# Kernel optimization log

Measured on AMD Instinct MI355X. Metric: run time of the kernel, lower is better.

Reference implementation:

```python
import jax, jax.numpy as jnp
import numpy as np

N = 100000       # nodes
E = 1600000      # edges
F_IN = 128       # input features
HID = 64         # hidden dim
CLS = 16         # classes


def setup_inputs() -> dict:
    key = jax.random.key(0)
    k = jax.random.split(key, 6)
    x = jax.random.normal(k[0], (N, F_IN), dtype=jnp.float32)
    src = jax.random.randint(k[1], (E,), 0, N, dtype=jnp.int32)
    dst = jax.random.randint(k[2], (E,), 0, N, dtype=jnp.int32)
    edge_index = jnp.stack([src, dst], axis=0)
    W1 = jax.random.normal(k[3], (F_IN, HID), dtype=jnp.float32) * (1.0 / np.sqrt(F_IN))
    b1 = jnp.zeros((HID,), dtype=jnp.float32)
    W2 = jax.random.normal(k[4], (HID, CLS), dtype=jnp.float32) * (1.0 / np.sqrt(HID))
    b2 = jnp.zeros((CLS,), dtype=jnp.float32)
    return {"x": x, "edge_index": edge_index, "W1": W1, "b1": b1, "W2": W2, "b2": b2}


def gcn_conv(x, W, b, src, dst, n_nodes):
    # GCNConv(normalize=True): h = W x; out_i = sum_{j->i} h_j / sqrt(d_i d_j) + h_i / d_i + b
    # (self-loops added with weight 1; deg includes the self-loop)
    h = x @ W                                             # [N, out]
    ones = jnp.ones(src.shape[0], dtype=x.dtype)
    deg = jax.ops.segment_sum(ones, dst, num_segments=n_nodes) + 1.0   # [N]
    dinv = deg ** -0.5
    norm = dinv[src] * dinv[dst]                          # [E]
    msg = h[src] * norm[:, None]                          # [E, out] gather
    out = jax.ops.segment_sum(msg, dst, num_segments=n_nodes)          # scatter-add
    out = out + h * (1.0 / deg)[:, None] + b              # self-loop term + bias
    return out


def reference(x, edge_index, W1, b1, W2, b2):
    src, dst = edge_index[0], edge_index[1]
    n = x.shape[0]
    h = jax.nn.relu(gcn_conv(x, W1, b1, src, dst, n))
    # dropout(p=0.5) is identity in eval mode
    h = jax.nn.relu(gcn_conv(h, W2, b2, src, dst, n))
    return jax.nn.log_softmax(h, axis=-1)
```

## Files before the change

kernel.cpp:

```cpp
#include <hip/hip_runtime.h>
#include <hip/hip_bf16.h>


typedef unsigned short u16;
typedef __attribute__((ext_vector_type(8))) short short8;
typedef __attribute__((ext_vector_type(4))) float f32x4;

#define CAP 4096

__device__ __forceinline__ float bf2f(u16 u) {
  return __uint_as_float(((unsigned int)u) << 16);
}
__device__ __forceinline__ u16 f2bf(float f) {
  unsigned int u = __float_as_uint(f);
  u += 0x7fffu + ((u >> 16) & 1u);
  return (u16)(u >> 16);
}
__device__ __forceinline__ float blo(unsigned int u) {
  return __uint_as_float(u << 16);
}
__device__ __forceinline__ float bhi(unsigned int u) {
  return __uint_as_float(u & 0xffff0000u);
}

__global__ __launch_bounds__(512) void kpartc(
    const int* __restrict__ src, const int* __restrict__ dst,
    int* __restrict__ cursor, int* __restrict__ etmp,
    const void* __restrict__ W1r, const void* __restrict__ b1r,
    const void* __restrict__ W2r, const void* __restrict__ b2r,
    u16* __restrict__ W1t, float* __restrict__ b1f, u16* __restrict__ W2b,
    float* __restrict__ b2f, int* __restrict__ mode, int E, int NB) {
  __shared__ int hist[1024], basep[1024];
  __shared__ float red[8];
  __shared__ int smode;
  int tid = threadIdx.x;

  if (blockIdx.x == 0) {
    const u16* w = (const u16*)W1r;
    float mx = 0.f;
    for (int i = tid; i < 8192; i += 512) {
      float av = fabsf(bf2f(w[i]));
      if (!(av <= 1e6f)) av = 3e38f;
      mx = fmaxf(mx, av);
    }
    #pragma unroll
    for (int off = 32; off >= 1; off >>= 1) mx = fmaxf(mx, __shfl_xor(mx, off, 64));
    if ((tid & 63) == 0) red[tid >> 6] = mx;
    __syncthreads();
    if (tid == 0) {
      float m2 = 0.f;
      #pragma unroll
      for (int wv = 0; wv < 8; ++wv) m2 = fmaxf(m2, red[wv]);
      smode = (m2 > 1e6f) ? 1 : 0;
      mode[0] = smode;
    }
    __syncthreads();
    int m = smode;
    for (int i = tid; i < 8192; i += 512) {
      int f = i >> 9, l = (i >> 3) & 63, j = i & 7;
      int k = (f >> 2) * 32 + (l >> 4) * 8 + j;
      int n = (f & 3) * 16 + (l & 15);
      int s = k * 64 + n;
      W1t[i] = m ? f2bf(((const float*)W1r)[s]) : ((const u16*)W1r)[s];
    }
    for (int i = tid; i < 1024; i += 512)
      W2b[i] = m ? f2bf(((const float*)W2r)[i]) : ((const u16*)W2r)[i];
    if (tid < 64) b1f[tid] = m ? ((const float*)b1r)[tid] : bf2f(((const u16*)b1r)[tid]);
    if (tid < 16) b2f[tid] = m ? ((const float*)b2r)[tid] : bf2f(((const u16*)b2r)[tid]);
    return;
  }

  for (int i = tid; i < 1024; i += 512) hist[i] = 0;
  __syncthreads();
  int e0 = (blockIdx.x - 1) * 8192 + tid * 16;
  int pk[16], off[16], cb[16];
  if (e0 + 15 < E) {
    int4 s4[4], d4[4];
    #pragma unroll
    for (int u = 0; u < 4; ++u) {
      s4[u] = ((const int4*)(src + e0))[u];
      d4[u] = ((const int4*)(dst + e0))[u];
    }
    const int* sp = (const int*)s4;
    const int* dp = (const int*)d4;
    #pragma unroll
    for (int k = 0; k < 16; ++k) {
      int s = sp[k], d = dp[k];
      cb[k] = d >> 7;
      pk[k] = (s << 7) | (d & 127);
      off[k] = atomicAdd(&hist[cb[k]], 1);
    }
  } else {
    #pragma unroll
    for (int k = 0; k < 16; ++k) {
      int e = e0 + k;
      cb[k] = -1;
      if (e < E) {
        int s = src[e], d = dst[e];
        cb[k] = d >> 7;
        pk[k] = (s << 7) | (d & 127);
        off[k] = atomicAdd(&hist[cb[k]], 1);
      }
    }
  }
  __syncthreads();
  for (int i = tid; i < NB; i += 512)
    if (hist[i]) basep[i] = atomicAdd(&cursor[i], hist[i]);
  __syncthreads();
  if (e0 + 15 < E) {
    #pragma unroll
    for (int k = 0; k < 16; ++k)
      etmp[cb[k] * CAP + basep[cb[k]] + off[k]] = pk[k];
  } else {
    #pragma unroll
    for (int k = 0; k < 16; ++k)
      if (cb[k] >= 0) etmp[cb[k] * CAP + basep[cb[k]] + off[k]] = pk[k];
  }
}

__global__ __launch_bounds__(256) void ksort(
    const int* __restrict__ etmp, const int* __restrict__ cursor,
    float* __restrict__ dinv, int* __restrict__ esort,
    int2* __restrict__ rowse, int N) {
  __shared__ int hist[128], curs[128];
  int tid = threadIdx.x;
  int bk = blockIdx.x;
  int base = bk * CAP;
  int cnt = cursor[bk];
  int node0 = bk << 7;

  if (tid < 128) hist[tid] = 0;
  __syncthreads();
  for (int i = tid; i < cnt; i += 256)
    atomicAdd(&hist[etmp[base + i] & 127], 1);
  __syncthreads();
  if (tid < 64) {
    int v0 = hist[tid], v1 = hist[tid + 64];
    int s0 = v0;
    #pragma unroll
    for (int off = 1; off < 64; off <<= 1) {
      int t = __shfl_up(s0, off, 64);
      if (tid >= off) s0 += t;
    }
    int tot0 = __shfl(s0, 63, 64);
    int s1 = v1;
    #pragma unroll
    for (int off = 1; off < 64; off <<= 1) {
      int t = __shfl_up(s1, off, 64);
      if (tid >= off) s1 += t;
    }
    s1 += tot0;
    int e0x = s0 - v0, e1x = s1 - v1;
    curs[tid] = e0x;
    curs[tid + 64] = e1x;
    int n0 = node0 + tid, n1 = n0 + 64;
    if (n0 < N) {
      rowse[n0] = make_int2(base + e0x, base + e0x + v0);
      dinv[n0] = rsqrtf((float)(v0 + 1));
    }
    if (n1 < N) {
      rowse[n1] = make_int2(base + e1x, base + e1x + v1);
      dinv[n1] = rsqrtf((float)(v1 + 1));
    }
  }
  __syncthreads();
  for (int i = tid; i < cnt; i += 256) {
    int pk = etmp[base + i];
    int pos = atomicAdd(&curs[pk & 127], 1);
    esort[base + pos] = pk >> 7;
  }
}

__global__ __launch_bounds__(256, 6) void kgemm1(
    const void* __restrict__ xraw, const u16* __restrict__ W1t,
    const int* __restrict__ mode, const float* __restrict__ dinv,
    u16* __restrict__ h1s, int N) {
  int tid = threadIdx.x;
  int mflag = mode[0];
  int lane = tid & 63, wv = tid >> 6;
  int m16 = lane & 15, q = lane >> 4;
  int row0 = blockIdx.x * 64 + wv * 16;

  f32x4 acc[4];
  #pragma unroll
  for (int jb = 0; jb < 4; ++jb) acc[jb] = (f32x4){0.f, 0.f, 0.f, 0.f};

  int rowm = row0 + m16;
  size_t rc = (size_t)((rowm < N) ? rowm : (N - 1));
  #pragma unroll
  for (int kb = 0; kb < 4; ++kb) {
    short8 a;
    if (mflag) {
      const float* xf = (const float*)xraw + rc * 128 + kb * 32 + q * 8;
      float4 u0 = ((const float4*)xf)[0];
      float4 u1 = ((const float4*)xf)[1];
      __hip_bfloat162 p0 = __float22bfloat162_rn(make_float2(u0.x, u0.y));
      __hip_bfloat162 p1 = __float22bfloat162_rn(make_float2(u0.z, u0.w));
      __hip_bfloat162 p2 = __float22bfloat162_rn(make_float2(u1.x, u1.y));
      __hip_bfloat162 p3 = __float22bfloat162_rn(make_float2(u1.z, u1.w));
      unsigned int w0 = *(const unsigned int*)&p0;
      unsigned int w1 = *(const unsigned int*)&p1;
      unsigned int w2 = *(const unsigned int*)&p2;
      unsigned int w3 = *(const unsigned int*)&p3;
      a[0] = (short)(w0 & 0xffff); a[1] = (short)(w0 >> 16);
      a[2] = (short)(w1 & 0xffff); a[3] = (short)(w1 >> 16);
      a[4] = (short)(w2 & 0xffff); a[5] = (short)(w2 >> 16);
      a[6] = (short)(w3 & 0xffff); a[7] = (short)(w3 >> 16);
    } else {
      a = *(const short8*)((const u16*)xraw + rc * 128 + kb * 32 + q * 8);
    }
    #pragma unroll
    for (int jb = 0; jb < 4; ++jb) {
      short8 bwf = *(const short8*)(W1t + (size_t)((kb * 4 + jb) * 64 + lane) * 8);
      acc[jb] = __builtin_amdgcn_mfma_f32_16x16x32_bf16(a, bwf, acc[jb], 0, 0, 0);
    }
  }

  int r4 = row0 + q * 4;
  float4 dvv = (r4 + 3 < N) ? *(const float4*)(dinv + r4)
                            : make_float4(0.f, 0.f, 0.f, 0.f);
  float dv[4] = {dvv.x, dvv.y, dvv.z, dvv.w};
  if (r4 + 3 >= N) {
    #pragma unroll
    for (int r = 0; r < 4; ++r) dv[r] = (r4 + r < N) ? dinv[r4 + r] : 0.f;
  }
  #pragma unroll
  for (int r = 0; r < 4; ++r) {
    int rr = r4 + r;
    if (rr < N) {
      #pragma unroll
      for (int jb = 0; jb < 4; ++jb)
        h1s[(size_t)rr * 64 + jb * 16 + m16] = f2bf(acc[jb][r] * dv[r]);
    }
  }
}

__global__ __launch_bounds__(256) void kagg1f(
    const u16* __restrict__ h1s, const int* __restrict__ esort,
    const int2* __restrict__ rowse, const float* __restrict__ dinv,
    const float* __restrict__ b1f, const u16* __restrict__ W2b,
    u16* __restrict__ h2sb, int N) {
  __shared__ __align__(16) u16 sA[4][16 * 72];
  __shared__ float sdv[4][16];
  int tid = threadIdx.x;
  int lane = tid & 63, wv = tid >> 6;
  int o = lane >> 3, fl = lane & 7;
  int wbase = blockIdx.x * 64 + wv * 16;

  const uint4* __restrict__ h1v4 = (const uint4*)h1s;

  #pragma unroll
  for (int sub = 0; sub < 2; ++sub) {
    int nloc = sub * 8 + o;
    int node = wbase + nloc;
    int cn = (node < N) ? node : (N - 1);
    int2 se = (node < N) ? rowse[node] : make_int2(0, 0);
    int beg = se.x, end = se.y;
    float a0 = 0.f, a1 = 0.f, a2 = 0.f, a3 = 0.f;
    float a4 = 0.f, a5 = 0.f, a6 = 0.f, a7 = 0.f;

    int k = beg;
    int myi = (k + 8 <= end) ? esort[k + fl] : 0;
    while (k + 8 <= end) {
      int cur = myi;
      if (k + 16 <= end) myi = esort[k + 8 + fl];
      uint4 g[8];
      #pragma unroll
      for (int p = 0; p < 8; ++p) {
        int s = __shfl(cur, (o << 3) + p, 64);
        g[p] = h1v4[s * 8 + fl];
      }
      #pragma unroll
      for (int p = 0; p < 8; ++p) {
        a0 += blo(g[p].x); a1 += bhi(g[p].x);
        a2 += blo(g[p].y); a3 += bhi(g[p].y);
        a4 += blo(g[p].z); a5 += bhi(g[p].z);
        a6 += blo(g[p].w); a7 += bhi(g[p].w);
      }
      k += 8;
    }
    for (; k < end; ++k) {
      int s = esort[k];
      uint4 g = h1v4[s * 8 + fl];
      a0 += blo(g.x); a1 += bhi(g.x);
      a2 += blo(g.y); a3 += bhi(g.y);
      a4 += blo(g.z); a5 += bhi(g.z);
      a6 += blo(g.w); a7 += bhi(g.w);
    }

    uint4 sg = h1v4[cn * 8 + fl];
    float dv = dinv[cn];
    float4 bva = ((const float4*)b1f)[fl * 2];
    float4 bvb = ((const float4*)b1f)[fl * 2 + 1];
    float v0 = fmaxf(dv * (a0 + blo(sg.x)) + bva.x, 0.f);
    float v1 = fmaxf(dv * (a1 + bhi(sg.x)) + bva.y, 0.f);
    float v2 = fmaxf(dv * (a2 + blo(sg.y)) + bva.z, 0.f);
    float v3 = fmaxf(dv * (a3 + bhi(sg.y)) + bva.w, 0.f);
    float v4 = fmaxf(dv * (a4 + blo(sg.z)) + bvb.x, 0.f);
    float v5 = fmaxf(dv * (a5 + bhi(sg.z)) + bvb.y, 0.f);
    float v6 = fmaxf(dv * (a6 + blo(sg.w)) + bvb.z, 0.f);
    float v7 = fmaxf(dv * (a7 + bhi(sg.w)) + bvb.w, 0.f);
    uint4 st;
    st.x = (unsigned int)f2bf(v0) | ((unsigned int)f2bf(v1) << 16);
    st.y = (unsigned int)f2bf(v2) | ((unsigned int)f2bf(v3) << 16);
    st.z = (unsigned int)f2bf(v4) | ((unsigned int)f2bf(v5) << 16);
    st.w = (unsigned int)f2bf(v6) | ((unsigned int)f2bf(v7) << 16);
    *(uint4*)&sA[wv][nloc * 72 + fl * 8] = st;
    if (fl == 0) sdv[wv][nloc] = dv;
  }

  int m16 = lane & 15, q = lane >> 4;
  short8 bw0, bw1;
  #pragma unroll
  for (int j = 0; j < 8; ++j) {
    bw0[j] = (short)W2b[(q * 8 + j) * 16 + m16];
    bw1[j] = (short)W2b[(32 + q * 8 + j) * 16 + m16];
  }
  __builtin_amdgcn_wave_barrier();

  const u16* ar = &sA[wv][m16 * 72];
  short8 af0 = *(const short8*)(ar + q * 8);
  short8 af1 = *(const short8*)(ar + 32 + q * 8);
  f32x4 c = (f32x4){0.f, 0.f, 0.f, 0.f};
  c = __builtin_amdgcn_mfma_f32_16x16x32_bf16(af0, bw0, c, 0, 0, 0);
  c = __builtin_amdgcn_mfma_f32_16x16x32_bf16(af1, bw1, c, 0, 0, 0);
  #pragma unroll
  for (int r = 0; r < 4; ++r) {
    int nloc2 = q * 4 + r;
    int nd2 = wbase + nloc2;
    if (nd2 < N) h2sb[(size_t)nd2 * 16 + m16] = f2bf(c[r] * sdv[wv][nloc2]);
  }
}

__global__ __launch_bounds__(256) void kagg2(
    const u16* __restrict__ h2sb, const int* __restrict__ esort,
    const int2* __restrict__ rowse, const float* __restrict__ dinv,
    const float* __restrict__ b2f, const int* __restrict__ mode,
    void* __restrict__ out, int n) {
  int mflag = mode[0];
  int tid = threadIdx.x;
  int lane = tid & 63, wv = tid >> 6;
  int oc = lane >> 3, ol = lane & 7;
  int hl = ol >> 2, fl = ol & 3;
  int node = blockIdx.x * 32 + wv * 8 + oc;
  if (node >= n) node = n - 1;
  int2 se = rowse[node];
  int beg = se.x, end = se.y;
  const uint2* h2v = (const uint2*)h2sb;
  uint2 sg = h2v[node * 4 + fl];
  float a0 = 0.f, a1 = 0.f, a2 = 0.f, a3 = 0.f;

  int k = beg;
  for (; k + 8 <= end; k += 8) {
    int i0 = esort[k + hl], i1 = esort[k + 2 + hl];
    int i2 = esort[k + 4 + hl], i3 = esort[k + 6 + hl];
    uint2 g0 = h2v[i0 * 4 + fl];
    uint2 g1 = h2v[i1 * 4 + fl];
    uint2 g2 = h2v[i2 * 4 + fl];
    uint2 g3 = h2v[i3 * 4 + fl];
    a0 += bf2f((u16)(g0.x & 0xffff)) + bf2f((u16)(g1.x & 0xffff))
        + bf2f((u16)(g2.x & 0xffff)) + bf2f((u16)(g3.x & 0xffff));
    a1 += bf2f((u16)(g0.x >> 16)) + bf2f((u16)(g1.x >> 16))
        + bf2f((u16)(g2.x >> 16)) + bf2f((u16)(g3.x >> 16));
    a2 += bf2f((u16)(g0.y & 0xffff)) + bf2f((u16)(g1.y & 0xffff))
        + bf2f((u16)(g2.y & 0xffff)) + bf2f((u16)(g3.y & 0xffff));
    a3 += bf2f((u16)(g0.y >> 16)) + bf2f((u16)(g1.y >> 16))
        + bf2f((u16)(g2.y >> 16)) + bf2f((u16)(g3.y >> 16));
  }
  for (; k < end; k += 2) {
    int e = k + hl;
    bool valid = e < end;
    uint2 g = h2v[esort[valid ? e : (end - 1)] * 4 + fl];
    if (valid) {
      a0 += bf2f((u16)(g.x & 0xffff));  a1 += bf2f((u16)(g.x >> 16));
      a2 += bf2f((u16)(g.y & 0xffff));  a3 += bf2f((u16)(g.y >> 16));
    }
  }
  a0 += __shfl_xor(a0, 4, 8);  a1 += __shfl_xor(a1, 4, 8);
  a2 += __shfl_xor(a2, 4, 8);  a3 += __shfl_xor(a3, 4, 8);

  float dv = dinv[node];
  float4 bv = ((const float4*)b2f)[fl];
  float v0 = fmaxf(dv * (a0 + bf2f((u16)(sg.x & 0xffff))) + bv.x, 0.f);
  float v1 = fmaxf(dv * (a1 + bf2f((u16)(sg.x >> 16))) + bv.y, 0.f);
  float v2 = fmaxf(dv * (a2 + bf2f((u16)(sg.y & 0xffff))) + bv.z, 0.f);
  float v3 = fmaxf(dv * (a3 + bf2f((u16)(sg.y >> 16))) + bv.w, 0.f);

  float m = fmaxf(fmaxf(v0, v1), fmaxf(v2, v3));
  m = fmaxf(m, __shfl_xor(m, 1, 4));
  m = fmaxf(m, __shfl_xor(m, 2, 4));
  float ex = __expf(v0 - m) + __expf(v1 - m) + __expf(v2 - m) + __expf(v3 - m);
  ex += __shfl_xor(ex, 1, 4);
  ex += __shfl_xor(ex, 2, 4);
  float lg = __logf(ex);
  float r0 = v0 - m - lg, r1 = v1 - m - lg;
  float r2 = v2 - m - lg, r3 = v3 - m - lg;
  if (hl == 0) {
    if (mflag) {
      ((float4*)out)[(size_t)node * 4 + fl] = make_float4(r0, r1, r2, r3);
    } else {
      uint2 o;
      o.x = (unsigned int)f2bf(r0) | ((unsigned int)f2bf(r1) << 16);
      o.y = (unsigned int)f2bf(r2) | ((unsigned int)f2bf(r3) << 16);
      ((uint2*)out)[(size_t)node * 4 + fl] = o;
    }
  }
}

extern "C" void kernel_launch(void* const* d_in, const int* in_sizes, int n_in,
                              void* d_out, int out_size, void* d_ws, size_t ws_size,
                              hipStream_t stream) {
  const void* x  = d_in[0];
  const int* ei  = (const int*)d_in[1];
  const void* W1 = d_in[2];
  const void* b1 = d_in[3];
  const void* W2 = d_in[4];
  const void* b2 = d_in[5];

  const int N = in_sizes[0] / 128;
  const int E = in_sizes[1] / 2;
  const int* src = ei;
  const int* dst = ei + E;
  const int NB = (N + 127) >> 7;

  char* ws = (char*)d_ws;
  size_t off = 0;
  auto alloc = [&](size_t bytes) -> char* {
    char* p = ws + off;
    off = (off + bytes + 255) & ~(size_t)255;
    return p;
  };
  u16*   h1s    = (u16*)  alloc((size_t)N * 64 * 2);
  u16*   h2sb   = (u16*)  alloc((size_t)N * 16 * 2);
  int*   etmp   = (int*)  alloc((size_t)NB * CAP * 4);
  int*   esort  = (int*)  alloc((size_t)NB * CAP * 4);
  int2*  rowse  = (int2*) alloc((size_t)N * 8);
  float* dinv   = (float*)alloc((size_t)N * 4);
  int*   cursor = (int*)  alloc((size_t)NB * 4);
  u16*   W1t    = (u16*)  alloc(8192 * 2);
  u16*   W2b    = (u16*)  alloc(1024 * 2);
  float* b1f    = (float*)alloc(64 * 4);
  float* b2f    = (float*)alloc(16 * 4);
  int*   mode   = (int*)  alloc(4);

  hipMemsetAsync(cursor, 0, (size_t)NB * 4, stream);

  int pblocks = (E + 8191) / 8192;
  kpartc<<<pblocks + 1, 512, 0, stream>>>(src, dst, cursor, etmp,
                                          W1, b1, W2, b2,
                                          W1t, b1f, W2b, b2f, mode, E, NB);
  ksort<<<NB, 256, 0, stream>>>(etmp, cursor, dinv, esort, rowse, N);
  kgemm1<<<(N + 63) / 64, 256, 0, stream>>>(x, W1t, mode, dinv, h1s, N);
  kagg1f<<<(N + 63) / 64, 256, 0, stream>>>(h1s, esort, rowse, dinv, b1f, W2b,
                                            h2sb, N);
  kagg2<<<(N + 31) / 32, 256, 0, stream>>>(h2sb, esort, rowse, dinv, b2f, mode,
                                           d_out, N);
}
```

Before: 190.3 us.

## Pad CSR rows to multiples of eight with zero-row sentinel, drop tail loops

Each node's sorted edge segment is padded up to a multiple of 8 with a sentinel index N that points to an extra all-zero row appended to h1s and h2sb. This lets both aggregation kernels drop their scalar remainder loops and run only the vectorized 8-edge loop, removing divergent tail work. The partition kernel also halves edges per thread (8 instead of 16) and doubles its block count. The padding adds wasted gathers of the zero row and can overflow CAP per bucket if padding pushes a bucket past capacity.

```diff
diff --git a/kernel.cpp b/kernel.cpp
--- a/kernel.cpp
+++ b/kernel.cpp
@@ -72,19 +72,19 @@
 
   for (int i = tid; i < 1024; i += 512) hist[i] = 0;
   __syncthreads();
-  int e0 = (blockIdx.x - 1) * 8192 + tid * 16;
-  int pk[16], off[16], cb[16];
-  if (e0 + 15 < E) {
-    int4 s4[4], d4[4];
-    #pragma unroll
-    for (int u = 0; u < 4; ++u) {
+  int e0 = (blockIdx.x - 1) * 4096 + tid * 8;
+  int pk[8], off[8], cb[8];
+  if (e0 + 7 < E) {
+    int4 s4[2], d4[2];
+    #pragma unroll
+    for (int u = 0; u < 2; ++u) {
       s4[u] = ((const int4*)(src + e0))[u];
       d4[u] = ((const int4*)(dst + e0))[u];
     }
     const int* sp = (const int*)s4;
     const int* dp = (const int*)d4;
     #pragma unroll
-    for (int k = 0; k < 16; ++k) {
+    for (int k = 0; k < 8; ++k) {
       int s = sp[k], d = dp[k];
       cb[k] = d >> 7;
       pk[k] = (s << 7) | (d & 127);
@@ -92,7 +92,7 @@
     }
   } else {
     #pragma unroll
-    for (int k = 0; k < 16; ++k) {
+    for (int k = 0; k < 8; ++k) {
       int e = e0 + k;
       cb[k] = -1;
       if (e < E) {
@@ -107,13 +107,13 @@
   for (int i = tid; i < NB; i += 512)
     if (hist[i]) basep[i] = atomicAdd(&cursor[i], hist[i]);
   __syncthreads();
-  if (e0 + 15 < E) {
-    #pragma unroll
-    for (int k = 0; k < 16; ++k)
+  if (e0 + 7 < E) {
+    #pragma unroll
+    for (int k = 0; k < 8; ++k)
       etmp[cb[k] * CAP + basep[cb[k]] + off[k]] = pk[k];
   } else {
     #pragma unroll
-    for (int k = 0; k < 16; ++k)
+    for (int k = 0; k < 8; ++k)
       if (cb[k] >= 0) etmp[cb[k] * CAP + basep[cb[k]] + off[k]] = pk[k];
   }
 }
@@ -121,14 +121,20 @@
 __global__ __launch_bounds__(256) void ksort(
     const int* __restrict__ etmp, const int* __restrict__ cursor,
     float* __restrict__ dinv, int* __restrict__ esort,
-    int2* __restrict__ rowse, int N) {
-  __shared__ int hist[128], curs[128];
+    int2* __restrict__ rowse, u16* __restrict__ h1s, u16* __restrict__ h2sb,
+    int N) {
+  __shared__ int hist[128], starts[128], curs[128];
   int tid = threadIdx.x;
   int bk = blockIdx.x;
   int base = bk * CAP;
   int cnt = cursor[bk];
   int node0 = bk << 7;
 
+  if (bk == 0) {
+    if (tid < 8) ((uint4*)h1s)[(size_t)N * 8 + tid] = make_uint4(0, 0, 0, 0);
+    if (tid < 2) ((uint4*)h2sb)[(size_t)N * 2 + tid] = make_uint4(0, 0, 0, 0);
+  }
+
   if (tid < 128) hist[tid] = 0;
   __syncthreads();
   for (int i = tid; i < cnt; i += 256)
@@ -136,34 +142,40 @@
   __syncthreads();
   if (tid < 64) {
     int v0 = hist[tid], v1 = hist[tid + 64];
-    int s0 = v0;
+    int p0 = (v0 + 7) & ~7, p1 = (v1 + 7) & ~7;
+    int s0 = p0;
     #pragma unroll
     for (int off = 1; off < 64; off <<= 1) {
       int t = __shfl_up(s0, off, 64);
       if (tid >= off) s0 += t;
     }
     int tot0 = __shfl(s0, 63, 64);
-    int s1 = v1;
+    int s1 = p1;
     #pragma unroll
     for (int off = 1; off < 64; off <<= 1) {
       int t = __shfl_up(s1, off, 64);
       if (tid >= off) s1 += t;
     }
     s1 += tot0;
-    int e0x = s0 - v0, e1x = s1 - v1;
-    curs[tid] = e0x;
-    curs[tid + 64] = e1x;
+    int st0 = s0 - p0, st1 = s1 - p1;
+    starts[tid] = st0;       starts[tid + 64] = st1;
+    curs[tid] = st0;         curs[tid + 64] = st1;
     int n0 = node0 + tid, n1 = n0 + 64;
     if (n0 < N) {
-      rowse[n0] = make_int2(base + e0x, base + e0x + v0);
+      rowse[n0] = make_int2(base + st0, base + st0 + p0);
       dinv[n0] = rsqrtf((float)(v0 + 1));
     }
     if (n1 < N) {
-      rowse[n1] = make_int2(base + e1x, base + e1x + v1);
+      rowse[n1] = make_int2(base + st1, base + st1 + p1);
       dinv[n1] = rsqrtf((float)(v1 + 1));
     }
   }
   __syncthreads();
+  if (tid < 128) {
+    int v = hist[tid], st = starts[tid];
+    int p = (v + 7) & ~7;
+    for (int j = v; j < p; ++j) esort[base + st + j] = N;
+  }
   for (int i = tid; i < cnt; i += 256) {
     int pk = etmp[base + i];
     int pos = atomicAdd(&curs[pk & 127], 1);
@@ -260,10 +272,11 @@
     float a4 = 0.f, a5 = 0.f, a6 = 0.f, a7 = 0.f;
 
     int k = beg;
-    int myi = (k + 8 <= end) ? esort[k + fl] : 0;
-    while (k + 8 <= end) {
+    int myi = (k < end) ? esort[k + fl] : 0;
+    while (k < end) {
       int cur = myi;
-      if (k + 16 <= end) myi = esort[k + 8 + fl];
+      int kn = k + 8;
+      if (kn < end) myi = esort[kn + fl];
       uint4 g[8];
       #pragma unroll
       for (int p = 0; p < 8; ++p) {
@@ -277,15 +290,7 @@
         a4 += blo(g[p].z); a5 += bhi(g[p].z);
         a6 += blo(g[p].w); a7 += bhi(g[p].w);
       }
-      k += 8;
-    }
-    for (; k < end; ++k) {
-      int s = esort[k];
-      uint4 g = h1v4[s * 8 + fl];
-      a0 += blo(g.x); a1 += bhi(g.x);
-      a2 += blo(g.y); a3 += bhi(g.y);
-      a4 += blo(g.z); a5 += bhi(g.z);
-      a6 += blo(g.w); a7 += bhi(g.w);
+      k = kn;
     }
 
     uint4 sg = h1v4[cn * 8 + fl];
@@ -350,8 +355,7 @@
   uint2 sg = h2v[node * 4 + fl];
   float a0 = 0.f, a1 = 0.f, a2 = 0.f, a3 = 0.f;
 
-  int k = beg;
-  for (; k + 8 <= end; k += 8) {
+  for (int k = beg; k < end; k += 8) {
     int i0 = esort[k + hl], i1 = esort[k + 2 + hl];
     int i2 = esort[k + 4 + hl], i3 = esort[k + 6 + hl];
     uint2 g0 = h2v[i0 * 4 + fl];
@@ -366,15 +370,6 @@
         + bf2f((u16)(g2.y & 0xffff)) + bf2f((u16)(g3.y & 0xffff));
     a3 += bf2f((u16)(g0.y >> 16)) + bf2f((u16)(g1.y >> 16))
         + bf2f((u16)(g2.y >> 16)) + bf2f((u16)(g3.y >> 16));
-  }
-  for (; k < end; k += 2) {
-    int e = k + hl;
-    bool valid = e < end;
-    uint2 g = h2v[esort[valid ? e : (end - 1)] * 4 + fl];
-    if (valid) {
-      a0 += bf2f((u16)(g.x & 0xffff));  a1 += bf2f((u16)(g.x >> 16));
-      a2 += bf2f((u16)(g.y & 0xffff));  a3 += bf2f((u16)(g.y >> 16));
-    }
   }
   a0 += __shfl_xor(a0, 4, 8);  a1 += __shfl_xor(a1, 4, 8);
   a2 += __shfl_xor(a2, 4, 8);  a3 += __shfl_xor(a3, 4, 8);
@@ -430,8 +425,8 @@
     off = (off + bytes + 255) & ~(size_t)255;
     return p;
   };
-  u16*   h1s    = (u16*)  alloc((size_t)N * 64 * 2);
-  u16*   h2sb   = (u16*)  alloc((size_t)N * 16 * 2);
+  u16*   h1s    = (u16*)  alloc((size_t)(N + 1) * 64 * 2);
+  u16*   h2sb   = (u16*)  alloc((size_t)(N + 1) * 16 * 2);
   int*   etmp   = (int*)  alloc((size_t)NB * CAP * 4);
   int*   esort  = (int*)  alloc((size_t)NB * CAP * 4);
   int2*  rowse  = (int2*) alloc((size_t)N * 8);
@@ -445,11 +440,12 @@
 
   hipMemsetAsync(cursor, 0, (size_t)NB * 4, stream);
 
-  int pblocks = (E + 8191) / 8192;
+  int pblocks = (E + 4095) / 4096;
   kpartc<<<pblocks + 1, 512, 0, stream>>>(src, dst, cursor, etmp,
                                           W1, b1, W2, b2,
                                           W1t, b1f, W2b, b2f, mode, E, NB);
-  ksort<<<NB, 256, 0, stream>>>(etmp, cursor, dinv, esort, rowse, N);
+  ksort<<<NB, 256, 0, stream>>>(etmp, cursor, dinv, esort, rowse,
+                                h1s, h2sb, N);
   kgemm1<<<(N + 63) / 64, 256, 0, stream>>>(x, W1t, mode, dinv, h1s, N);
   kagg1f<<<(N + 63) / 64, 256, 0, stream>>>(h1s, esort, rowse, dinv, b1f, W2b,
                                             h2sb, N);
```

New measurement: 188.6 us. About the same (-0.9%).
